# Performance work log

Measured on AMD Instinct MI355X. Metric: run time of the kernel, lower is better.

Reference implementation:

```python
import jax, jax.numpy as jnp
import numpy as np

B, SEQ, PRED = 128, 336, 24
I, H = 64, 256  # input_dim, hidden_dim; bidirectional, num_layers=1


def _lstm_dir(x, h0, c0, Wih, Whh, bih, bhh):
    # x: (B, T, F). torch gate order: i, f, g, o. Returns (hs (B,T,H), h_T, c_T).
    def step(carry, xt):
        h, c = carry
        g = xt @ Wih.T + h @ Whh.T + bih + bhh  # (B, 4H)
        gi, gf, gg, go = jnp.split(g, 4, axis=-1)
        c = jax.nn.sigmoid(gf) * c + jax.nn.sigmoid(gi) * jnp.tanh(gg)
        h = jax.nn.sigmoid(go) * jnp.tanh(c)
        return (h, c), h
    (hT, cT), hs = jax.lax.scan(step, (h0, c0), jnp.swapaxes(x, 0, 1))
    return jnp.swapaxes(hs, 0, 1), hT, cT


def _bilstm(x, h0, c0, Wih, Whh, bih, bhh):
    # h0, c0: (2, B, H) in torch layout [fwd, bwd]; Wih: (2, 4H, F) etc.
    hf, hF, cF = _lstm_dir(x, h0[0], c0[0], Wih[0], Whh[0], bih[0], bhh[0])
    hb, hB, cB = _lstm_dir(x[:, ::-1], h0[1], c0[1], Wih[1], Whh[1], bih[1], bhh[1])
    hb = hb[:, ::-1]
    out = jnp.concatenate([hf, hb], axis=-1)  # (B, T, 2H)
    return out, jnp.stack([hF, hB]), jnp.stack([cF, cB])


def setup_inputs() -> dict:
    key = jax.random.key(0)
    ks = jax.random.split(key, 12)
    s = 0.05
    return {
        "x": jax.random.normal(ks[0], (B, SEQ, I), dtype=jnp.float32),
        "enc_Wih": jax.random.normal(ks[1], (2, 4 * H, I), dtype=jnp.float32) * s,
        "enc_Whh": jax.random.normal(ks[2], (2, 4 * H, H), dtype=jnp.float32) * s,
        "enc_bih": jax.random.normal(ks[3], (2, 4 * H), dtype=jnp.float32) * s,
        "enc_bhh": jax.random.normal(ks[4], (2, 4 * H), dtype=jnp.float32) * s,
        "dec_Wih": jax.random.normal(ks[5], (2, 4 * H, I), dtype=jnp.float32) * s,
        "dec_Whh": jax.random.normal(ks[6], (2, 4 * H, H), dtype=jnp.float32) * s,
        "dec_bih": jax.random.normal(ks[7], (2, 4 * H), dtype=jnp.float32) * s,
        "dec_bhh": jax.random.normal(ks[8], (2, 4 * H), dtype=jnp.float32) * s,
        "lin_W": jax.random.normal(ks[9], (I, 2 * H), dtype=jnp.float32) * s,
        "lin_b": jax.random.normal(ks[10], (I,), dtype=jnp.float32) * s,
    }


def reference(x, enc_Wih, enc_Whh, enc_bih, enc_bhh,
              dec_Wih, dec_Whh, dec_bih, dec_bhh, lin_W, lin_b):
    zeros = jnp.zeros((2, x.shape[0], H), dtype=x.dtype)
    # encoder over full input sequence
    _, h, c = _bilstm(x, zeros, zeros, enc_Wih, enc_Whh, enc_bih, enc_bhh)
    dec_in = x[:, -1:, :]
    outs = []
    for t in range(PRED):
        lstm_out, h, c = _bilstm(dec_in, h, c, dec_Wih, dec_Whh, dec_bih, dec_bhh)
        feat = jnp.concatenate([lstm_out[:, -1, :H], lstm_out[:, 0, H:]], axis=-1)
        y = feat @ lin_W.T + lin_b  # (B, I)
        outs.append(y)
        dec_in = jnp.stack(outs, axis=1)  # (B, t+1, I)
    return jnp.stack(outs, axis=1)  # (B, PRED, I)
```

## Files before the change

### kernel.cpp

```cpp
#include <hip/hip_runtime.h>

#define BB    128
#define SEQL  336
#define PREDN 24
#define IN    64
#define HH    256
#define GG    1024
#define KTOT  320
#define NBLK  256

__device__ float g_wt_enc[2 * KTOT * GG];
__device__ float g_wt_dec[2 * KTOT * GG];
__device__ float g_linwt[2 * HH * IN];
__device__ float g_bs_enc[2 * GG];
__device__ float g_bs_dec[2 * GG];
__device__ float g_linb[IN];
__device__ float g_h[2][2 * BB * HH];
__device__ float g_ys[PREDN * BB * IN];
__device__ int   g_flag[NBLK * 16];

#define N_WT   (2 * KTOT * GG)
#define N_PREP (2 * N_WT + 2 * HH * IN + 4 * GG + IN + 2 * 2 * BB * HH + PREDN * BB * IN + NBLK * 16)

__global__ void prep_kernel(const float* __restrict__ eWih,
                            const float* __restrict__ eWhh,
                            const float* __restrict__ ebih,
                            const float* __restrict__ ebhh,
                            const float* __restrict__ dWih,
                            const float* __restrict__ dWhh,
                            const float* __restrict__ dbih,
                            const float* __restrict__ dbhh,
                            const float* __restrict__ linW,
                            const float* __restrict__ linb)
{
    int idx = blockIdx.x * 256 + threadIdx.x;
    if (idx >= N_PREP) return;

    if (idx < N_WT) {
        int d  = idx / (KTOT * GG);
        int r2 = idx % (KTOT * GG);
        int k  = r2 / GG;
        int q  = r2 % GG;
        int nn = q >> 2, g = q & 3;
        int j  = g * HH + nn;
        g_wt_enc[idx] = (k < IN) ? eWih[(d * GG + j) * IN + k]
                                 : eWhh[(d * GG + j) * HH + (k - IN)];
        return;
    }
    idx -= N_WT;
    if (idx < N_WT) {
        int d  = idx / (KTOT * GG);
        int r2 = idx % (KTOT * GG);
        int k  = r2 / GG;
        int q  = r2 % GG;
        int nn = q >> 2, g = q & 3;
        int j  = g * HH + nn;
        g_wt_dec[idx] = (k < IN) ? dWih[(d * GG + j) * IN + k]
                                 : dWhh[(d * GG + j) * HH + (k - IN)];
        return;
    }
    idx -= N_WT;
    if (idx < 2 * HH * IN) {
        int k = idx / IN, o = idx % IN;
        g_linwt[idx] = linW[o * (2 * HH) + k];
        return;
    }
    idx -= 2 * HH * IN;
    if (idx < 2 * GG) { g_bs_enc[idx] = ebih[idx] + ebhh[idx]; return; }
    idx -= 2 * GG;
    if (idx < 2 * GG) { g_bs_dec[idx] = dbih[idx] + dbhh[idx]; return; }
    idx -= 2 * GG;
    if (idx < IN) { g_linb[idx] = linb[idx]; return; }
    idx -= IN;
    if (idx < 2 * 2 * BB * HH) { ((float*)g_h)[idx] = 0.0f; return; }
    idx -= 2 * 2 * BB * HH;
    if (idx < PREDN * BB * IN) { g_ys[idx] = 0.0f; return; }
    idx -= PREDN * BB * IN;
    if (idx < NBLK * 16) { g_flag[idx] = 0; return; }
}

__device__ __forceinline__ float sigm(float v) { return 1.0f / (1.0f + expf(-v)); }

__device__ __forceinline__ float agent_ld(const float* p) {
    return __hip_atomic_load(p, __ATOMIC_RELAXED, __HIP_MEMORY_SCOPE_AGENT);
}
__device__ __forceinline__ void agent_st(float* p, float v) {
    __hip_atomic_store(p, v, __ATOMIC_RELAXED, __HIP_MEMORY_SCOPE_AGENT);
}

__global__ __launch_bounds__(256)
void lstm_main(const float* __restrict__ x, float* __restrict__ out)
{
    __shared__ float4 w4[KTOT * 16];
    __shared__ __align__(16) float um[16 * 516];
    __shared__ float part[16 * 16 * 2];

    const int tid   = threadIdx.x;
    const int blk   = blockIdx.x;
    const int dir   = blk >> 7;
    const int btile = (blk >> 4) & 7;
    const int ntile = blk & 15;
    const int nl    = tid & 15;
    const int bl    = tid >> 4;
    const int n0    = ntile * 16;
    const int b0    = btile * 16;
    const int n     = n0 + nl;
    const int b     = b0 + bl;

    int* myflag = &g_flag[blk * 16];
    int  ev = 0;

    auto sync_g = [&](int nwait) {
        ++ev;
        __atomic_signal_fence(__ATOMIC_SEQ_CST);
        __builtin_amdgcn_s_waitcnt(0);
        __atomic_signal_fence(__ATOMIC_SEQ_CST);
        __syncthreads();
        if (tid == 0)
            __hip_atomic_store(myflag, ev, __ATOMIC_RELAXED, __HIP_MEMORY_SCOPE_AGENT);
        if (tid < nwait) {
            int d = (nwait == 32) ? (tid >> 4) : dir;
            int m = tid & 15;
            int* f = &g_flag[(((d << 3) | btile) * 16 + m) * 16];
            while (__hip_atomic_load(f, __ATOMIC_RELAXED, __HIP_MEMORY_SCOPE_AGENT) < ev)
                __builtin_amdgcn_s_sleep(1);
        }
        __atomic_signal_fence(__ATOMIC_SEQ_CST);
        __syncthreads();
    };

    float4 bias;
    auto load_w = [&](const float* wsrc, const float* bsrc) {
        const float4* w4g = (const float4*)wsrc + dir * (KTOT * 256);
        for (int i = tid; i < KTOT * 16; i += 256) {
            int k = i >> 4, nn = i & 15;
            w4[i] = w4g[k * 256 + n0 + nn];
        }
        const float* bs = bsrc + dir * GG;
        bias = make_float4(bs[n], bs[256 + n], bs[512 + n], bs[768 + n]);
        __syncthreads();
    };

    float c = 0.0f;
    int   p = 0;

    auto step = [&](int mode, int tval, int L) {
        float* hsrc = g_h[p];
        float4 xv;
        float  yv[4];
        if (mode <= 1) {
            int bl2 = tid >> 4, j = tid & 15;
            int te = (mode == 0) ? (dir ? (SEQL - 1 - tval) : tval) : (SEQL - 1);
            xv = ((const float4*)(x + ((b0 + bl2) * SEQL + te) * IN))[j];
        } else {
            int e = dir ? (L - 1 - tval) : tval;
            #pragma unroll
            for (int jj = 0; jj < 4; ++jj) {
                int i = tid + jj * 256;
                int bl2 = i >> 6, j = i & 63;
                yv[jj] = agent_ld(g_ys + (e * BB + b0 + bl2) * IN + j);
            }
        }
        float rh[16];
        #pragma unroll
        for (int jj = 0; jj < 16; ++jj)
            rh[jj] = agent_ld(hsrc + (dir * BB + b0 + jj) * HH + tid);

        if (mode <= 1) {
            int bl2 = tid >> 4, j = tid & 15;
            *(float4*)&um[bl2 * 516 + 4 * j] = xv;
        } else {
            #pragma unroll
            for (int jj = 0; jj < 4; ++jj) {
                int i = tid + jj * 256;
                int bl2 = i >> 6, j = i & 63;
                um[bl2 * 516 + j] = yv[jj];
            }
        }
        #pragma unroll
        for (int jj = 0; jj < 16; ++jj)
            um[jj * 516 + IN + tid] = rh[jj];
        __syncthreads();

        float a0 = bias.x, a1 = bias.y, a2 = bias.z, a3 = bias.w;
        const float* arow = &um[bl * 516];
        #pragma unroll 4
        for (int k4 = 0; k4 < KTOT / 4; ++k4) {
            float4 av = *(const float4*)&arow[4 * k4];
            float4 w0 = w4[(4 * k4 + 0) * 16 + nl];
            float4 w1 = w4[(4 * k4 + 1) * 16 + nl];
            float4 w2 = w4[(4 * k4 + 2) * 16 + nl];
            float4 w3 = w4[(4 * k4 + 3) * 16 + nl];
            a0 = fmaf(av.x, w0.x, a0); a1 = fmaf(av.x, w0.y, a1); a2 = fmaf(av.x, w0.z, a2); a3 = fmaf(av.x, w0.w, a3);
            a0 = fmaf(av.y, w1.x, a0); a1 = fmaf(av.y, w1.y, a1); a2 = fmaf(av.y, w1.z, a2); a3 = fmaf(av.y, w1.w, a3);
            a0 = fmaf(av.z, w2.x, a0); a1 = fmaf(av.z, w2.y, a1); a2 = fmaf(av.z, w2.z, a2); a3 = fmaf(av.z, w2.w, a3);
            a0 = fmaf(av.w, w3.x, a0); a1 = fmaf(av.w, w3.y, a1); a2 = fmaf(av.w, w3.z, a2); a3 = fmaf(av.w, w3.w, a3);
        }
        float ig = sigm(a0);
        float fg = sigm(a1);
        float gt = tanhf(a2);
        float og = sigm(a3);
        c = fg * c + ig * gt;
        float hn = og * tanhf(c);
        agent_st(&g_h[p ^ 1][(dir * BB + b) * HH + n], hn);
        p ^= 1;
    };

    load_w(g_wt_enc, g_bs_enc);
    for (int t = 0; t < SEQL; ++t) { step(0, t, 0); sync_g(16); }

    load_w(g_wt_dec, g_bs_dec);

    for (int t = 0; t < PREDN; ++t) {
        int L = t ? t : 1;
        for (int s = 0; s < L; ++s) {
            step((t == 0) ? 1 : 2, s, L);
            sync_g((s == L - 1) ? 32 : 16);
        }
        {
            float* hc = g_h[p];
            float rh2[32];
            #pragma unroll
            for (int jj = 0; jj < 32; ++jj) {
                int i = tid + jj * 256;
                int bl2 = i >> 9, j = i & 511;
                const float* base = (j < 256) ? (hc + (b0 + bl2) * HH + j)
                                              : (hc + (BB + b0 + bl2) * HH + (j - 256));
                rh2[jj] = agent_ld(base);
            }
            #pragma unroll
            for (int jj = 0; jj < 32; ++jj) {
                int i = tid + jj * 256;
                int bl2 = i >> 9, j = i & 511;
                um[bl2 * 516 + j] = rh2[jj];
            }
            __syncthreads();
            int bl2 = tid >> 4, ks = tid & 15;
            int o0  = ((dir << 4) | ntile) << 1;
            float p0 = 0.0f, p1 = 0.0f;
            const float* hr = &um[bl2 * 516 + ks * 32];
            const float* lw = g_linwt + (ks * 32) * IN + o0;
            #pragma unroll 8
            for (int j = 0; j < 32; ++j) {
                float hv = hr[j];
                p0 = fmaf(hv, lw[j * IN],     p0);
                p1 = fmaf(hv, lw[j * IN + 1], p1);
            }
            part[(bl2 * 16 + ks) * 2]     = p0;
            part[(bl2 * 16 + ks) * 2 + 1] = p1;
            __syncthreads();
            if (tid < 32) {
                int b2 = tid >> 1, oi = tid & 1;
                float acc = g_linb[o0 + oi];
                #pragma unroll
                for (int m2 = 0; m2 < 16; ++m2) acc += part[(b2 * 16 + m2) * 2 + oi];
                agent_st(&g_ys[(t * BB + b0 + b2) * IN + o0 + oi], acc);
                out[(b0 + b2) * (PREDN * IN) + t * IN + o0 + oi] = acc;
            }
            sync_g(32);
        }
    }
}

extern "C" void kernel_launch(void* const* d_in, const int* in_sizes, int n_in,
                              void* d_out, int out_size, void* d_ws, size_t ws_size,
                              hipStream_t stream)
{
    (void)in_sizes; (void)n_in; (void)out_size; (void)d_ws; (void)ws_size;
    const float* x    = (const float*)d_in[0];
    const float* eWih = (const float*)d_in[1];
    const float* eWhh = (const float*)d_in[2];
    const float* ebih = (const float*)d_in[3];
    const float* ebhh = (const float*)d_in[4];
    const float* dWih = (const float*)d_in[5];
    const float* dWhh = (const float*)d_in[6];
    const float* dbih = (const float*)d_in[7];
    const float* dbhh = (const float*)d_in[8];
    const float* linW = (const float*)d_in[9];
    const float* linb = (const float*)d_in[10];
    float* out = (float*)d_out;

    int prep_blocks = (N_PREP + 255) / 256;
    hipLaunchKernelGGL(prep_kernel, dim3(prep_blocks), dim3(256), 0, stream,
                       eWih, eWhh, ebih, ebhh, dWih, dWhh, dbih, dbhh, linW, linb);

    void* args[] = { (void*)&x, (void*)&out };
    (void)hipLaunchCooperativeKernel((void*)lstm_main, dim3(NBLK), dim3(256), args, 0, stream);
}
```

Before: 3.852 ms.

## Compute LSTM gate GEMM with split-bf16 MFMA instead of fp32 FMA

Weights are pre-split into bf16 hi/lo pairs, and each step's inputs and hidden state are split the same way. The per-step gate matmul then runs as three 16x16x32 bf16 MFMAs per k-chunk (hi*hi, hi*lo, lo*hi), one wave per gate, replacing the per-thread fp32 FMA loop. Gate results go through shared memory so each thread can apply the cell update. This is meant to shorten the compute part of the latency-bound recurrent step. In exchange it adds split/convert work on every step, an extra barrier, and a small precision loss from dropping the lo*lo term.

```diff
diff --git a/kernel.cpp b/kernel.cpp
--- a/kernel.cpp
+++ b/kernel.cpp
@@ -9,8 +9,15 @@
 #define KTOT  320
 #define NBLK  256
 
-__device__ float g_wt_enc[2 * KTOT * GG];
-__device__ float g_wt_dec[2 * KTOT * GG];
+typedef unsigned int  uint_t;
+typedef unsigned short ush;
+using s8v = __attribute__((ext_vector_type(8))) short;
+using f4v = __attribute__((ext_vector_type(4))) float;
+
+__device__ ush   g_webh[2 * 4 * 256 * KTOT];
+__device__ ush   g_webl[2 * 4 * 256 * KTOT];
+__device__ ush   g_wdbh[2 * 4 * 256 * KTOT];
+__device__ ush   g_wdbl[2 * 4 * 256 * KTOT];
 __device__ float g_linwt[2 * HH * IN];
 __device__ float g_bs_enc[2 * GG];
 __device__ float g_bs_dec[2 * GG];
@@ -19,8 +26,17 @@
 __device__ float g_ys[PREDN * BB * IN];
 __device__ int   g_flag[NBLK * 16];
 
-#define N_WT   (2 * KTOT * GG)
+#define N_WT   (2 * 4 * 256 * KTOT)
 #define N_PREP (2 * N_WT + 2 * HH * IN + 4 * GG + IN + 2 * 2 * BB * HH + PREDN * BB * IN + NBLK * 16)
+
+__device__ __forceinline__ void bfsplit(float v, uint_t& hi, uint_t& lo) {
+    uint_t u = __float_as_uint(v);
+    uint_t h = (u + 0x7FFFu + ((u >> 16) & 1u)) >> 16;
+    float  r = v - __uint_as_float(h << 16);
+    uint_t u2 = __float_as_uint(r);
+    uint_t l = (u2 + 0x7FFFu + ((u2 >> 16) & 1u)) >> 16;
+    hi = h; lo = l;
+}
 
 __global__ void prep_kernel(const float* __restrict__ eWih,
                             const float* __restrict__ eWhh,
@@ -37,26 +53,30 @@
     if (idx >= N_PREP) return;
 
     if (idx < N_WT) {
-        int d  = idx / (KTOT * GG);
-        int r2 = idx % (KTOT * GG);
-        int k  = r2 / GG;
-        int q  = r2 % GG;
-        int nn = q >> 2, g = q & 3;
-        int j  = g * HH + nn;
-        g_wt_enc[idx] = (k < IN) ? eWih[(d * GG + j) * IN + k]
-                                 : eWhh[(d * GG + j) * HH + (k - IN)];
+        int d   = idx / (4 * 256 * KTOT);
+        int sub = idx % (4 * 256 * KTOT);
+        int g   = sub / (256 * KTOT);
+        int n2  = (sub / KTOT) % 256;
+        int k   = sub % KTOT;
+        int j   = g * HH + n2;
+        float v = (k < IN) ? eWih[(d * GG + j) * IN + k]
+                           : eWhh[(d * GG + j) * HH + (k - IN)];
+        uint_t hi, lo; bfsplit(v, hi, lo);
+        g_webh[idx] = (ush)hi; g_webl[idx] = (ush)lo;
         return;
     }
     idx -= N_WT;
     if (idx < N_WT) {
-        int d  = idx / (KTOT * GG);
-        int r2 = idx % (KTOT * GG);
-        int k  = r2 / GG;
-        int q  = r2 % GG;
-        int nn = q >> 2, g = q & 3;
-        int j  = g * HH + nn;
-        g_wt_dec[idx] = (k < IN) ? dWih[(d * GG + j) * IN + k]
-                                 : dWhh[(d * GG + j) * HH + (k - IN)];
+        int d   = idx / (4 * 256 * KTOT);
+        int sub = idx % (4 * 256 * KTOT);
+        int g   = sub / (256 * KTOT);
+        int n2  = (sub / KTOT) % 256;
+        int k   = sub % KTOT;
+        int j   = g * HH + n2;
+        float v = (k < IN) ? dWih[(d * GG + j) * IN + k]
+                           : dWhh[(d * GG + j) * HH + (k - IN)];
+        uint_t hi, lo; bfsplit(v, hi, lo);
+        g_wdbh[idx] = (ush)hi; g_wdbl[idx] = (ush)lo;
         return;
     }
     idx -= N_WT;
@@ -91,8 +111,12 @@
 __global__ __launch_bounds__(256)
 void lstm_main(const float* __restrict__ x, float* __restrict__ out)
 {
-    __shared__ float4 w4[KTOT * 16];
-    __shared__ __align__(16) float um[16 * 516];
+    __shared__ __align__(16) ush  sAh[10 * 64 * 8];
+    __shared__ __align__(16) ush  sAl[10 * 64 * 8];
+    __shared__ __align__(16) ush  sBh[4 * 10 * 64 * 8];
+    __shared__ __align__(16) ush  sBl[4 * 10 * 64 * 8];
+    __shared__ float gbuf[4 * 16 * 16];
+    __shared__ float um[16 * 516];
     __shared__ float part[16 * 16 * 2];
 
     const int tid   = threadIdx.x;
@@ -106,6 +130,8 @@
     const int b0    = btile * 16;
     const int n     = n0 + nl;
     const int b     = b0 + bl;
+    const int lane  = tid & 63;
+    const int wave  = tid >> 6;
 
     int* myflag = &g_flag[blk * 16];
     int  ev = 0;
@@ -129,15 +155,22 @@
         __syncthreads();
     };
 
-    float4 bias;
-    auto load_w = [&](const float* wsrc, const float* bsrc) {
-        const float4* w4g = (const float4*)wsrc + dir * (KTOT * 256);
-        for (int i = tid; i < KTOT * 16; i += 256) {
-            int k = i >> 4, nn = i & 15;
-            w4[i] = w4g[k * 256 + n0 + nn];
-        }
-        const float* bs = bsrc + dir * GG;
-        bias = make_float4(bs[n], bs[256 + n], bs[512 + n], bs[768 + n]);
+    float bw;
+    auto load_w = [&](const ush* wh, const ush* wl, const float* bsrc) {
+        wh += dir * (4 * 256 * KTOT);
+        wl += dir * (4 * 256 * KTOT);
+        for (int i = tid; i < 4 * 16 * 80; i += 256) {
+            int g   = i / (16 * 80);
+            int r   = i % (16 * 80);
+            int nl_ = r / 80;
+            int k   = (r % 80) * 4;
+            int src = ((g * 256) + n0 + nl_) * KTOT + k;
+            int kc = k >> 5, quad = (k & 31) >> 3, j = k & 7;
+            int dst = ((g * 10 + kc) * 64 + quad * 16 + nl_) * 8 + j;
+            *(uint2*)&sBh[dst] = *(const uint2*)(wh + src);
+            *(uint2*)&sBl[dst] = *(const uint2*)(wl + src);
+        }
+        bw = bsrc[dir * GG + wave * HH + n0 + (lane & 15)];
         __syncthreads();
     };
 
@@ -146,70 +179,91 @@
 
     auto step = [&](int mode, int tval, int L) {
         float* hsrc = g_h[p];
-        float4 xv;
-        float  yv[4];
         if (mode <= 1) {
-            int bl2 = tid >> 4, j = tid & 15;
+            int xb = tid >> 4, xj = tid & 15;
             int te = (mode == 0) ? (dir ? (SEQL - 1 - tval) : tval) : (SEQL - 1);
-            xv = ((const float4*)(x + ((b0 + bl2) * SEQL + te) * IN))[j];
+            float4 xv = ((const float4*)(x + ((b0 + xb) * SEQL + te) * IN))[xj];
+            uint_t h0,l0,h1,l1,h2,l2,h3,l3;
+            bfsplit(xv.x,h0,l0); bfsplit(xv.y,h1,l1); bfsplit(xv.z,h2,l2); bfsplit(xv.w,h3,l3);
+            int k = 4 * xj;
+            int base = (((k >> 5) * 64 + ((k & 31) >> 3) * 16 + xb) * 8) + (k & 7);
+            *(uint_t*)&sAh[base]     = h0 | (h1 << 16);
+            *(uint_t*)&sAh[base + 2] = h2 | (h3 << 16);
+            *(uint_t*)&sAl[base]     = l0 | (l1 << 16);
+            *(uint_t*)&sAl[base + 2] = l2 | (l3 << 16);
         } else {
             int e = dir ? (L - 1 - tval) : tval;
+            float yv[4];
             #pragma unroll
             for (int jj = 0; jj < 4; ++jj) {
                 int i = tid + jj * 256;
-                int bl2 = i >> 6, j = i & 63;
-                yv[jj] = agent_ld(g_ys + (e * BB + b0 + bl2) * IN + j);
-            }
-        }
-        float rh[16];
-        #pragma unroll
-        for (int jj = 0; jj < 16; ++jj)
-            rh[jj] = agent_ld(hsrc + (dir * BB + b0 + jj) * HH + tid);
-
-        if (mode <= 1) {
-            int bl2 = tid >> 4, j = tid & 15;
-            *(float4*)&um[bl2 * 516 + 4 * j] = xv;
-        } else {
+                yv[jj] = agent_ld(g_ys + (e * BB + b0 + (i >> 6)) * IN + (i & 63));
+            }
             #pragma unroll
             for (int jj = 0; jj < 4; ++jj) {
                 int i = tid + jj * 256;
-                int bl2 = i >> 6, j = i & 63;
-                um[bl2 * 516 + j] = yv[jj];
-            }
-        }
+                int yb = i >> 6, k = i & 63;
+                uint_t hi, lo; bfsplit(yv[jj], hi, lo);
+                int base = (((k >> 5) * 64 + ((k & 31) >> 3) * 16 + yb) * 8) + (k & 7);
+                sAh[base] = (ush)hi; sAl[base] = (ush)lo;
+            }
+        }
+        {
+            int hb = tid & 15, cblk = tid >> 4;
+            const float* hp = hsrc + (dir * BB + b0 + hb) * HH + cblk * 16;
+            float rh[16];
+            #pragma unroll
+            for (int m = 0; m < 16; ++m) rh[m] = agent_ld(hp + m);
+            #pragma unroll
+            for (int m = 0; m < 16; m += 2) {
+                int k = IN + cblk * 16 + m;
+                uint_t h0,l0,h1,l1;
+                bfsplit(rh[m], h0, l0); bfsplit(rh[m+1], h1, l1);
+                int base = (((k >> 5) * 64 + ((k & 31) >> 3) * 16 + hb) * 8) + (k & 7);
+                *(uint_t*)&sAh[base] = h0 | (h1 << 16);
+                *(uint_t*)&sAl[base] = l0 | (l1 << 16);
+            }
+        }
+        __syncthreads();
+
+        f4v acc = { bw, bw, bw, bw };
+        const s8v* pAh = (const s8v*)sAh;
+        const s8v* pAl = (const s8v*)sAl;
+        const s8v* pBh = (const s8v*)sBh + wave * 10 * 64;
+        const s8v* pBl = (const s8v*)sBl + wave * 10 * 64;
         #pragma unroll
-        for (int jj = 0; jj < 16; ++jj)
-            um[jj * 516 + IN + tid] = rh[jj];
-        __syncthreads();
-
-        float a0 = bias.x, a1 = bias.y, a2 = bias.z, a3 = bias.w;
-        const float* arow = &um[bl * 516];
-        #pragma unroll 4
-        for (int k4 = 0; k4 < KTOT / 4; ++k4) {
-            float4 av = *(const float4*)&arow[4 * k4];
-            float4 w0 = w4[(4 * k4 + 0) * 16 + nl];
-            float4 w1 = w4[(4 * k4 + 1) * 16 + nl];
-            float4 w2 = w4[(4 * k4 + 2) * 16 + nl];
-            float4 w3 = w4[(4 * k4 + 3) * 16 + nl];
-            a0 = fmaf(av.x, w0.x, a0); a1 = fmaf(av.x, w0.y, a1); a2 = fmaf(av.x, w0.z, a2); a3 = fmaf(av.x, w0.w, a3);
-            a0 = fmaf(av.y, w1.x, a0); a1 = fmaf(av.y, w1.y, a1); a2 = fmaf(av.y, w1.z, a2); a3 = fmaf(av.y, w1.w, a3);
-            a0 = fmaf(av.z, w2.x, a0); a1 = fmaf(av.z, w2.y, a1); a2 = fmaf(av.z, w2.z, a2); a3 = fmaf(av.z, w2.w, a3);
-            a0 = fmaf(av.w, w3.x, a0); a1 = fmaf(av.w, w3.y, a1); a2 = fmaf(av.w, w3.z, a2); a3 = fmaf(av.w, w3.w, a3);
-        }
-        float ig = sigm(a0);
-        float fg = sigm(a1);
-        float gt = tanhf(a2);
-        float og = sigm(a3);
-        c = fg * c + ig * gt;
-        float hn = og * tanhf(c);
-        agent_st(&g_h[p ^ 1][(dir * BB + b) * HH + n], hn);
+        for (int kc = 0; kc < 10; ++kc) {
+            s8v ah = pAh[kc * 64 + lane];
+            s8v al = pAl[kc * 64 + lane];
+            s8v bh = pBh[kc * 64 + lane];
+            s8v blo = pBl[kc * 64 + lane];
+            acc = __builtin_amdgcn_mfma_f32_16x16x32_bf16(ah, bh,  acc, 0, 0, 0);
+            acc = __builtin_amdgcn_mfma_f32_16x16x32_bf16(ah, blo, acc, 0, 0, 0);
+            acc = __builtin_amdgcn_mfma_f32_16x16x32_bf16(al, bh,  acc, 0, 0, 0);
+        }
+        {
+            int quad = lane >> 4, ncol = lane & 15;
+            #pragma unroll
+            for (int r2 = 0; r2 < 4; ++r2)
+                gbuf[(wave * 16 + quad * 4 + r2) * 16 + ncol] = acc[r2];
+        }
+        __syncthreads();
+        {
+            float gi_ = gbuf[(0 * 16 + bl) * 16 + nl];
+            float gf_ = gbuf[(1 * 16 + bl) * 16 + nl];
+            float gg_ = gbuf[(2 * 16 + bl) * 16 + nl];
+            float go_ = gbuf[(3 * 16 + bl) * 16 + nl];
+            c = sigm(gf_) * c + sigm(gi_) * tanhf(gg_);
+            float hn = sigm(go_) * tanhf(c);
+            agent_st(&g_h[p ^ 1][(dir * BB + b) * HH + n], hn);
+        }
         p ^= 1;
     };
 
-    load_w(g_wt_enc, g_bs_enc);
+    load_w(g_webh, g_webl, g_bs_enc);
     for (int t = 0; t < SEQL; ++t) { step(0, t, 0); sync_g(16); }
 
-    load_w(g_wt_dec, g_bs_dec);
+    load_w(g_wdbh, g_wdbl, g_bs_dec);
 
     for (int t = 0; t < PREDN; ++t) {
         int L = t ? t : 1;
@@ -251,11 +305,11 @@
             __syncthreads();
             if (tid < 32) {
                 int b2 = tid >> 1, oi = tid & 1;
-                float acc = g_linb[o0 + oi];
+                float acc2 = g_linb[o0 + oi];
                 #pragma unroll
-                for (int m2 = 0; m2 < 16; ++m2) acc += part[(b2 * 16 + m2) * 2 + oi];
-                agent_st(&g_ys[(t * BB + b0 + b2) * IN + o0 + oi], acc);
-                out[(b0 + b2) * (PREDN * IN) + t * IN + o0 + oi] = acc;
+                for (int m2 = 0; m2 < 16; ++m2) acc2 += part[(b2 * 16 + m2) * 2 + oi];
+                agent_st(&g_ys[(t * BB + b0 + b2) * IN + o0 + oi], acc2);
+                out[(b0 + b2) * (PREDN * IN) + t * IN + o0 + oi] = acc2;
             }
             sync_g(32);
         }
```

New measurement: 3.410 ms. -11.5%, faster.
